# Performance work log

Hardware: AMD Instinct MI355X
Metric: run time of the kernel (lower is better)

Reference implementation:

```python
import jax, jax.numpy as jnp
import numpy as np
from jax import lax

B, C_IN, HC, H, W, K = 32, 32, 64, 64, 64, 3


def _conv(x, w, b):
    # x: [B,C,H,W], w: [O,I,K,K] -> [B,O,H,W] (stride 1, pad 1)
    y = lax.conv_general_dilated(x, w, window_strides=(1, 1), padding=[(1, 1), (1, 1)],
                                 dimension_numbers=("NCHW", "OIHW", "NCHW"))
    return y + b[None, :, None, None]


def setup_inputs() -> dict:
    key = jax.random.key(0)
    ks = jax.random.split(key, 20)
    d = {
        "x": jax.random.normal(ks[0], (B, C_IN, H, W), jnp.float32),
        "hidden_state": jax.random.normal(ks[1], (B, HC, H, W), jnp.float32),
        "cell_state": jax.random.normal(ks[2], (B, HC, H, W), jnp.float32),
    }
    sx = 1.0 / np.sqrt(C_IN * K * K)
    sh = 1.0 / np.sqrt(HC * K * K)
    names_x = ["w_xi", "w_xf", "w_xo", "w_xg"]
    names_h = ["w_hi", "w_hf", "w_ho", "w_hg"]
    for i, n in enumerate(names_x):
        d[n] = jax.random.uniform(ks[3 + i], (HC, C_IN, K, K), jnp.float32, -sx, sx)
        d["b" + n[1:]] = jax.random.uniform(ks[7 + i], (HC,), jnp.float32, -sx, sx)
    for i, n in enumerate(names_h):
        d[n] = jax.random.uniform(ks[11 + i], (HC, HC, K, K), jnp.float32, -sh, sh)
        d["b" + n[1:]] = jax.random.uniform(ks[15 + i], (HC,), jnp.float32, -sh, sh)
    return d


def reference(x, hidden_state, cell_state,
              w_xi, w_xf, w_xo, w_xg, b_xi, b_xf, b_xo, b_xg,
              w_hi, w_hf, w_ho, w_hg, b_hi, b_hf, b_ho, b_hg):
    Wx = jnp.concatenate([w_xi, w_xf, w_xo, w_xg], axis=0)
    bx = jnp.concatenate([b_xi, b_xf, b_xo, b_xg], axis=0)
    Wh = jnp.concatenate([w_hi, w_hf, w_ho, w_hg], axis=0)
    bh = jnp.concatenate([b_hi, b_hf, b_ho, b_hg], axis=0)
    gates = _conv(x, Wx, bx) + _conv(hidden_state, Wh, bh)  # [B,4*HC,H,W]
    zi, zf, zo, zg = jnp.split(gates, 4, axis=1)
    i = jax.nn.sigmoid(zi)
    f = jax.nn.sigmoid(zf)
    o = jax.nn.sigmoid(zo)
    g = jnp.tanh(zg)
    c_new = f * cell_state + i * g
    h_new = o * jnp.tanh(c_new)
    return (h_new, c_new)
```

## Files before the change

### kernel.cpp

```cpp
#include <hip/hip_runtime.h>


#define B_   32
#define CIN  32
#define HC_  64
#define HH   64
#define WW   64

#define A_ELEMS (9 * 6 * 8 * 64 * 8)
#define P_ROW   (12 * 66 * 8)
#define AKK     4096
#define BLDS    25344

typedef __attribute__((ext_vector_type(8)))  short  short8;
typedef __attribute__((ext_vector_type(16))) float  floatx16;

struct PackArgs {
    const float* wx[4]; const float* wh[4];
    const float* bx[4]; const float* bh[4];
};

__device__ __forceinline__ short f2bf(float f) {
    unsigned u = __float_as_uint(f);
    u += 0x7FFFu + ((u >> 16) & 1u);
    return (short)(u >> 16);
}

__device__ __forceinline__ void gl_lds16(const short* g, short* l) {
    __builtin_amdgcn_global_load_lds(
        (const __attribute__((address_space(1))) unsigned int*)g,
        (__attribute__((address_space(3))) unsigned int*)l, 16, 0, 0);
}

__global__ __launch_bounds__(256) void pack_weights(PackArgs pa, short* a_pk, float* bias) {
    int idx = blockIdx.x * 256 + threadIdx.x;
    if (idx < A_ELEMS) {
        int j    = idx & 7;
        int lane = (idx >> 3) & 63;
        int rest = idx >> 9;
        int s    = rest & 7;
        int rest2 = rest >> 3;
        int kk   = rest2 % 6;
        int tap  = rest2 / 6;
        int og = s >> 1, fi = s & 1;
        int m32 = lane & 31;
        int gate = 2 * fi + (m32 >> 4);
        int oc   = og * 16 + (m32 & 15);
        int c    = kk * 16 + (lane >> 5) * 8 + j;
        int ky = tap / 3, kx = tap - 3 * ky;
        float v = (c < CIN)
            ? pa.wx[gate][((oc * CIN + c) * 3 + ky) * 3 + kx]
            : pa.wh[gate][((oc * HC_ + (c - CIN)) * 3 + ky) * 3 + kx];
        a_pk[idx] = f2bf(v);
    }
    if (idx < 256) {
        int gate = idx >> 6, oc = idx & 63;
        bias[idx] = pa.bx[gate][oc] + pa.bh[gate][oc];
    }
}

__global__ __launch_bounds__(256) void pack_input(const float* __restrict__ x,
                                                  const float* __restrict__ h,
                                                  short* __restrict__ P) {
    const int yy = blockIdx.x, b = blockIdx.y;
    int4* prow4 = (int4*)(P + ((size_t)b * 66 + yy) * P_ROW);

    if (yy == 0 || yy == 65) {
        int4 z = {0, 0, 0, 0};
        for (int g = threadIdx.x; g < 792; g += 256) prow4[g] = z;
        return;
    }

    __shared__ short t[64 * 98];
    const int y = yy - 1;
    const int col = threadIdx.x & 63, cg = threadIdx.x >> 6;
    for (int c = cg; c < 96; c += 4) {
        float v = (c < CIN) ? x[((b * CIN + c) * HH + y) * WW + col]
                            : h[((b * HC_ + (c - CIN)) * HH + y) * WW + col];
        t[col * 98 + c] = f2bf(v);
    }
    __syncthreads();

    for (int g = threadIdx.x; g < 792; g += 256) {
        int pc = g / 66, xx = g - 66 * pc;
        int4 val = {0, 0, 0, 0};
        if (xx >= 1 && xx <= 64) {
            const short* sp = &t[(xx - 1) * 98 + pc * 8];
            val.x = *(const int*)(sp + 0); val.y = *(const int*)(sp + 2);
            val.z = *(const int*)(sp + 4); val.w = *(const int*)(sp + 6);
        }
        prow4[g] = val;
    }
}

__global__ __launch_bounds__(512, 4) void convlstm_main(
    const short* __restrict__ P, const short* __restrict__ a_pk,
    const float* __restrict__ bias, const float* __restrict__ cell,
    float* __restrict__ out)
{
    __shared__ __align__(16) short lds[BLDS];

    const int tid = threadIdx.x;
    const int b  = blockIdx.x >> 5;
    const int y0 = (blockIdx.x & 31) * 2;

    const int wv = tid >> 6, lane = tid & 63;
    const int ln31 = lane & 31, hg = lane >> 5;
    const int og = wv & 3, nh = wv >> 2;
    const int y = y0 + nh;

    floatx16 acc[2][2];
    #pragma unroll
    for (int fi = 0; fi < 2; ++fi)
        #pragma unroll
        for (int ns = 0; ns < 2; ++ns)
            #pragma unroll
            for (int q = 0; q < 16; ++q) acc[fi][ns][q] = 0.f;

    const short* Ag  = a_pk + og * 1024 + lane * 8;
    const int    b_rd = nh * 6336 + hg * 528 + ln31 * 8;

    {
        const short* Bsrc = P + ((size_t)(b * 66) + y0) * P_ROW;
        #pragma unroll
        for (int i = 0; i < 7; ++i) {
            int id = i * 512 + tid;
            if (id < 3168)
                gl_lds16(Bsrc + id * 8, lds + (i * 512 + wv * 64) * 8);
        }
    }
    __syncthreads();

    for (int tap = 0; tap < 9; ++tap) {
        const int ky = tap / 3, kx = tap % 3;
        const short* Bb = lds + b_rd + ky * 6336 + kx * 8;
        const short* Ac = Ag + tap * 6 * AKK;

        #pragma unroll
        for (int kk = 0; kk < 6; ++kk) {
            short8 a0 = *(const short8*)&Ac[kk * AKK];
            short8 a1 = *(const short8*)&Ac[kk * AKK + 512];
            short8 b0 = *(const short8*)&Bb[kk * 1056];
            short8 b1 = *(const short8*)&Bb[kk * 1056 + 256];
            acc[0][0] = __builtin_amdgcn_mfma_f32_32x32x16_bf16(a0, b0, acc[0][0], 0, 0, 0);
            acc[0][1] = __builtin_amdgcn_mfma_f32_32x32x16_bf16(a0, b1, acc[0][1], 0, 0, 0);
            acc[1][0] = __builtin_amdgcn_mfma_f32_32x32x16_bf16(a1, b0, acc[1][0], 0, 0, 0);
            acc[1][1] = __builtin_amdgcn_mfma_f32_32x32x16_bf16(a1, b1, acc[1][1], 0, 0, 0);
        }
    }

    const size_t plane = (size_t)B_ * HC_ * HH * WW;
    #pragma unroll
    for (int q = 0; q < 4; ++q)
    #pragma unroll
    for (int b8 = 0; b8 < 2; ++b8) {
        const int oc16 = q + 4 * hg + 8 * b8;
        const int oc = og * 16 + oc16;
        const float Bi = bias[oc],       Bf = bias[64 + oc];
        const float Bo = bias[128 + oc], Bg = bias[192 + oc];
        const int r_lo = q + 4 * b8, r_hi = q + 4 * (2 + b8);
        #pragma unroll
        for (int ns = 0; ns < 2; ++ns) {
            float zi = acc[0][ns][r_lo] + Bi;
            float zf = acc[0][ns][r_hi] + Bf;
            float zo = acc[1][ns][r_lo] + Bo;
            float zg = acc[1][ns][r_hi] + Bg;
            float ig = 1.f / (1.f + __expf(-zi));
            float fg = 1.f / (1.f + __expf(-zf));
            float sg = 1.f / (1.f + __expf(-zo));
            float e2 = __expf(2.f * zg);
            float gg = 1.f - 2.f / (e2 + 1.f);
            const int x = ns * 32 + ln31;
            size_t off = ((size_t)(b * HC_ + oc) * HH + y) * WW + x;
            float cn = fg * cell[off] + ig * gg;
            float ec = __expf(2.f * cn);
            out[off] = sg * (1.f - 2.f / (ec + 1.f));
            out[plane + off] = cn;
        }
    }
}

extern "C" void kernel_launch(void* const* d_in, const int* in_sizes, int n_in,
                              void* d_out, int out_size, void* d_ws, size_t ws_size,
                              hipStream_t stream) {
    PackArgs pa;
    pa.wx[0] = (const float*)d_in[3];  pa.bx[0] = (const float*)d_in[4];
    pa.wx[1] = (const float*)d_in[5];  pa.bx[1] = (const float*)d_in[6];
    pa.wx[2] = (const float*)d_in[7];  pa.bx[2] = (const float*)d_in[8];
    pa.wx[3] = (const float*)d_in[9];  pa.bx[3] = (const float*)d_in[10];
    pa.wh[0] = (const float*)d_in[11]; pa.bh[0] = (const float*)d_in[12];
    pa.wh[1] = (const float*)d_in[13]; pa.bh[1] = (const float*)d_in[14];
    pa.wh[2] = (const float*)d_in[15]; pa.bh[2] = (const float*)d_in[16];
    pa.wh[3] = (const float*)d_in[17]; pa.bh[3] = (const float*)d_in[18];

    short* a_pk = (short*)d_ws;
    float* bias = (float*)((char*)d_ws + A_ELEMS * sizeof(short));
    short* P    = (short*)((char*)d_ws + 443392);

    pack_weights<<<dim3(A_ELEMS / 256), dim3(256), 0, stream>>>(pa, a_pk, bias);
    pack_input <<<dim3(66, B_), dim3(256), 0, stream>>>(
        (const float*)d_in[0], (const float*)d_in[1], P);
    convlstm_main<<<dim3(B_ * 32), dim3(512), 0, stream>>>(
        P, a_pk, bias, (const float*)d_in[2], (float*)d_out);
}
```

Measured before the change: 245.8 us.

## Stage weights through triple-buffered LDS and stream input rows per kernel row

```diff
diff --git a/kernel.cpp b/kernel.cpp
--- a/kernel.cpp
+++ b/kernel.cpp
@@ -9,8 +9,8 @@
 
 #define A_ELEMS (9 * 6 * 8 * 64 * 8)
 #define P_ROW   (12 * 66 * 8)
-#define AKK     4096
-#define BLDS    25344
+#define ACH     8192
+#define BROWS   12672
 
 typedef __attribute__((ext_vector_type(8)))  short  short8;
 typedef __attribute__((ext_vector_type(16))) float  floatx16;
@@ -98,7 +98,7 @@
     const float* __restrict__ bias, const float* __restrict__ cell,
     float* __restrict__ out)
 {
-    __shared__ __align__(16) short lds[BLDS];
+    __shared__ __align__(16) short lds[BROWS + 3 * ACH];
 
     const int tid = threadIdx.x;
     const int b  = blockIdx.x >> 5;
@@ -117,37 +117,76 @@
             #pragma unroll
             for (int q = 0; q < 16; ++q) acc[fi][ns][q] = 0.f;
 
-    const short* Ag  = a_pk + og * 1024 + lane * 8;
-    const int    b_rd = nh * 6336 + hg * 528 + ln31 * 8;
-
-    {
-        const short* Bsrc = P + ((size_t)(b * 66) + y0) * P_ROW;
+    short* ldsB = lds;
+    short* As   = lds + BROWS;
+
+    const int a_rd = og * 1024 + lane * 8;
+    const int b_rd = nh * 6336 + hg * 528 + ln31 * 8;
+
+    #define STAGE_B(KY) do {                                                   \
+        const short* Bs_ = P + ((size_t)(b * 66) + y0 + (KY)) * P_ROW;         \
+        _Pragma("unroll")                                                      \
+        for (int i_ = 0; i_ < 3; ++i_)                                         \
+            gl_lds16(Bs_ + (i_ * 512 + tid) * 8, ldsB + (i_ * 512 + wv * 64) * 8); \
+        if (tid >= 464)                                                        \
+            gl_lds16(Bs_ + (1520 + lane) * 8, ldsB + 1520 * 8);                \
+    } while (0)
+
+    #define STAGE_A(C) do {                                                    \
+        const short* s_ = a_pk + (C) * ACH;                                    \
+        short* d_ = As + ((C) % 3) * ACH;                                      \
+        _Pragma("unroll")                                                      \
+        for (int i_ = 0; i_ < 2; ++i_)                                         \
+            gl_lds16(s_ + (i_ * 512 + tid) * 8, d_ + (i_ * 512 + wv * 64) * 8);\
+    } while (0)
+
+    STAGE_B(0);
+    STAGE_A(0);
+    STAGE_A(1);
+    asm volatile("s_waitcnt vmcnt(2)" ::: "memory");
+    __builtin_amdgcn_s_barrier();
+    __builtin_amdgcn_sched_barrier(0);
+
+    #pragma unroll
+    for (int c = 0; c < 27; ++c) {
+        const int tap = c / 3, ky = tap / 3, kx = tap % 3;
+        const bool bdry = (c == 9 || c == 18);
+
+        if (bdry) STAGE_B(ky);
+        if (c < 25) STAGE_A(c + 2);
+        if (bdry) {
+            asm volatile("s_waitcnt vmcnt(2)" ::: "memory");
+            __builtin_amdgcn_s_barrier();
+            __builtin_amdgcn_sched_barrier(0);
+        }
+
+        const short* Ab = As + (c % 3) * ACH + a_rd;
+        const short* Bb = ldsB + b_rd + kx * 8;
+
         #pragma unroll
-        for (int i = 0; i < 7; ++i) {
-            int id = i * 512 + tid;
-            if (id < 3168)
-                gl_lds16(Bsrc + id * 8, lds + (i * 512 + wv * 64) * 8);
-        }
-    }
-    __syncthreads();
-
-    for (int tap = 0; tap < 9; ++tap) {
-        const int ky = tap / 3, kx = tap % 3;
-        const short* Bb = lds + b_rd + ky * 6336 + kx * 8;
-        const short* Ac = Ag + tap * 6 * AKK;
-
-        #pragma unroll
-        for (int kk = 0; kk < 6; ++kk) {
-            short8 a0 = *(const short8*)&Ac[kk * AKK];
-            short8 a1 = *(const short8*)&Ac[kk * AKK + 512];
+        for (int kkl = 0; kkl < 2; ++kkl) {
+            const int kk = 2 * (c % 3) + kkl;
+            short8 a0 = *(const short8*)&Ab[kkl * 4096];
+            short8 a1 = *(const short8*)&Ab[kkl * 4096 + 512];
             short8 b0 = *(const short8*)&Bb[kk * 1056];
             short8 b1 = *(const short8*)&Bb[kk * 1056 + 256];
+            __builtin_amdgcn_s_setprio(1);
             acc[0][0] = __builtin_amdgcn_mfma_f32_32x32x16_bf16(a0, b0, acc[0][0], 0, 0, 0);
             acc[0][1] = __builtin_amdgcn_mfma_f32_32x32x16_bf16(a0, b1, acc[0][1], 0, 0, 0);
             acc[1][0] = __builtin_amdgcn_mfma_f32_32x32x16_bf16(a1, b0, acc[1][0], 0, 0, 0);
             acc[1][1] = __builtin_amdgcn_mfma_f32_32x32x16_bf16(a1, b1, acc[1][1], 0, 0, 0);
-        }
-    }
+            __builtin_amdgcn_s_setprio(0);
+        }
+
+        if (c < 25)       asm volatile("s_waitcnt vmcnt(2)" ::: "memory");
+        else if (c == 25) asm volatile("s_waitcnt vmcnt(0)" ::: "memory");
+        if (c < 26) {
+            __builtin_amdgcn_s_barrier();
+            __builtin_amdgcn_sched_barrier(0);
+        }
+    }
+    #undef STAGE_A
+    #undef STAGE_B
 
     const size_t plane = (size_t)B_ * HC_ * HH * WW;
     #pragma unroll
```

Measured after the change: 227.0 us. 7.6% less time.

## Stream weights through per-wave LDS ring with async loads; one row per block

Applied to the files above, without the earlier changes.

```diff
diff --git a/kernel.cpp b/kernel.cpp
--- a/kernel.cpp
+++ b/kernel.cpp
@@ -9,8 +9,8 @@
 
 #define A_ELEMS (9 * 6 * 8 * 64 * 8)
 #define P_ROW   (12 * 66 * 8)
-#define AKK     4096
-#define BLDS    25344
+#define BLDS    (3 * P_ROW)
+#define ARING   1024
 
 typedef __attribute__((ext_vector_type(8)))  short  short8;
 typedef __attribute__((ext_vector_type(16))) float  floatx16;
@@ -93,21 +93,20 @@
     }
 }
 
-__global__ __launch_bounds__(512, 4) void convlstm_main(
+__global__ __launch_bounds__(256, 2) void convlstm_main(
     const short* __restrict__ P, const short* __restrict__ a_pk,
     const float* __restrict__ bias, const float* __restrict__ cell,
     float* __restrict__ out)
 {
-    __shared__ __align__(16) short lds[BLDS];
+    __shared__ __align__(16) short lds[BLDS + 4 * 4 * ARING];
 
     const int tid = threadIdx.x;
-    const int b  = blockIdx.x >> 5;
-    const int y0 = (blockIdx.x & 31) * 2;
+    const int b = blockIdx.x >> 6;
+    const int y = blockIdx.x & 63;
 
     const int wv = tid >> 6, lane = tid & 63;
     const int ln31 = lane & 31, hg = lane >> 5;
-    const int og = wv & 3, nh = wv >> 2;
-    const int y = y0 + nh;
+    const int og = wv;
 
     floatx16 acc[2][2];
     #pragma unroll
@@ -117,36 +116,57 @@
             #pragma unroll
             for (int q = 0; q < 16; ++q) acc[fi][ns][q] = 0.f;
 
-    const short* Ag  = a_pk + og * 1024 + lane * 8;
-    const int    b_rd = nh * 6336 + hg * 528 + ln31 * 8;
+    short* Aring = lds + BLDS + wv * (4 * ARING);
+    const int b_rd = hg * 528 + ln31 * 8;
 
     {
-        const short* Bsrc = P + ((size_t)(b * 66) + y0) * P_ROW;
-        #pragma unroll
-        for (int i = 0; i < 7; ++i) {
-            int id = i * 512 + tid;
-            if (id < 3168)
-                gl_lds16(Bsrc + id * 8, lds + (i * 512 + wv * 64) * 8);
+        const short* Bsrc = P + ((size_t)(b * 66) + y) * P_ROW;
+        #pragma unroll
+        for (int i = 0; i < 10; ++i) {
+            int id = i * 256 + tid;
+            if (id < 2376)
+                gl_lds16(Bsrc + id * 8, lds + (i * 256 + wv * 64) * 8);
+        }
+        #pragma unroll
+        for (int ck = 0; ck < 3; ++ck) {
+            const short* src = a_pk + ck * 4096 + og * 1024 + lane * 8;
+            gl_lds16(src,       Aring + ck * ARING);
+            gl_lds16(src + 512, Aring + ck * ARING + 512);
         }
     }
     __syncthreads();
 
-    for (int tap = 0; tap < 9; ++tap) {
+    #pragma unroll
+    for (int c = 0; c < 54; ++c) {
+        const int tap = c / 6, kk = c % 6;
         const int ky = tap / 3, kx = tap % 3;
-        const short* Bb = lds + b_rd + ky * 6336 + kx * 8;
-        const short* Ac = Ag + tap * 6 * AKK;
-
-        #pragma unroll
-        for (int kk = 0; kk < 6; ++kk) {
-            short8 a0 = *(const short8*)&Ac[kk * AKK];
-            short8 a1 = *(const short8*)&Ac[kk * AKK + 512];
-            short8 b0 = *(const short8*)&Bb[kk * 1056];
-            short8 b1 = *(const short8*)&Bb[kk * 1056 + 256];
-            acc[0][0] = __builtin_amdgcn_mfma_f32_32x32x16_bf16(a0, b0, acc[0][0], 0, 0, 0);
-            acc[0][1] = __builtin_amdgcn_mfma_f32_32x32x16_bf16(a0, b1, acc[0][1], 0, 0, 0);
-            acc[1][0] = __builtin_amdgcn_mfma_f32_32x32x16_bf16(a1, b0, acc[1][0], 0, 0, 0);
-            acc[1][1] = __builtin_amdgcn_mfma_f32_32x32x16_bf16(a1, b1, acc[1][1], 0, 0, 0);
-        }
+
+        if (c < 51) {
+            const short* src = a_pk + (c + 3) * 4096 + og * 1024 + lane * 8;
+            short* dst = Aring + ((c + 3) & 3) * ARING;
+            gl_lds16(src,       dst);
+            gl_lds16(src + 512, dst + 512);
+        }
+
+        if (c < 51)       asm volatile("s_waitcnt vmcnt(6)" ::: "memory");
+        else if (c == 51) asm volatile("s_waitcnt vmcnt(4)" ::: "memory");
+        else if (c == 52) asm volatile("s_waitcnt vmcnt(2)" ::: "memory");
+        else              asm volatile("s_waitcnt vmcnt(0)" ::: "memory");
+
+        const short* Ab = Aring + (c & 3) * ARING + lane * 8;
+        const short* Bb = lds + b_rd + ky * 6336 + kk * 1056 + kx * 8;
+
+        short8 a0 = *(const short8*)&Ab[0];
+        short8 a1 = *(const short8*)&Ab[512];
+        short8 b0 = *(const short8*)&Bb[0];
+        short8 b1 = *(const short8*)&Bb[256];
+
+        __builtin_amdgcn_s_setprio(1);
+        acc[0][0] = __builtin_amdgcn_mfma_f32_32x32x16_bf16(a0, b0, acc[0][0], 0, 0, 0);
+        acc[0][1] = __builtin_amdgcn_mfma_f32_32x32x16_bf16(a0, b1, acc[0][1], 0, 0, 0);
+        acc[1][0] = __builtin_amdgcn_mfma_f32_32x32x16_bf16(a1, b0, acc[1][0], 0, 0, 0);
+        acc[1][1] = __builtin_amdgcn_mfma_f32_32x32x16_bf16(a1, b1, acc[1][1], 0, 0, 0);
+        __builtin_amdgcn_s_setprio(0);
     }
 
     const size_t plane = (size_t)B_ * HC_ * HH * WW;
@@ -200,6 +220,6 @@
     pack_weights<<<dim3(A_ELEMS / 256), dim3(256), 0, stream>>>(pa, a_pk, bias);
     pack_input <<<dim3(66, B_), dim3(256), 0, stream>>>(
         (const float*)d_in[0], (const float*)d_in[1], P);
-    convlstm_main<<<dim3(B_ * 32), dim3(512), 0, stream>>>(
+    convlstm_main<<<dim3(B_ * 64), dim3(256), 0, stream>>>(
         P, a_pk, bias, (const float*)d_in[2], (float*)d_out);
 }
```

New measurement: 226.9 us. 7.7% less time.

## Merge packing kernels and software-pipeline weight loads in the conv main loop

Applied to the files above, without the earlier changes.

```diff
diff --git a/kernel.cpp b/kernel.cpp
--- a/kernel.cpp
+++ b/kernel.cpp
@@ -9,8 +9,7 @@
 
 #define A_ELEMS (9 * 6 * 8 * 64 * 8)
 #define P_ROW   (12 * 66 * 8)
-#define AKK     4096
-#define BLDS    25344
+#define BLDS    (4 * P_ROW)
 
 typedef __attribute__((ext_vector_type(8)))  short  short8;
 typedef __attribute__((ext_vector_type(16))) float  floatx16;
@@ -32,37 +31,42 @@
         (__attribute__((address_space(3))) unsigned int*)l, 16, 0, 0);
 }
 
-__global__ __launch_bounds__(256) void pack_weights(PackArgs pa, short* a_pk, float* bias) {
-    int idx = blockIdx.x * 256 + threadIdx.x;
-    if (idx < A_ELEMS) {
-        int j    = idx & 7;
-        int lane = (idx >> 3) & 63;
-        int rest = idx >> 9;
-        int s    = rest & 7;
-        int rest2 = rest >> 3;
-        int kk   = rest2 % 6;
-        int tap  = rest2 / 6;
-        int og = s >> 1, fi = s & 1;
-        int m32 = lane & 31;
-        int gate = 2 * fi + (m32 >> 4);
-        int oc   = og * 16 + (m32 & 15);
-        int c    = kk * 16 + (lane >> 5) * 8 + j;
-        int ky = tap / 3, kx = tap - 3 * ky;
-        float v = (c < CIN)
-            ? pa.wx[gate][((oc * CIN + c) * 3 + ky) * 3 + kx]
-            : pa.wh[gate][((oc * HC_ + (c - CIN)) * 3 + ky) * 3 + kx];
-        a_pk[idx] = f2bf(v);
-    }
-    if (idx < 256) {
-        int gate = idx >> 6, oc = idx & 63;
-        bias[idx] = pa.bx[gate][oc] + pa.bh[gate][oc];
-    }
-}
-
-__global__ __launch_bounds__(256) void pack_input(const float* __restrict__ x,
-                                                  const float* __restrict__ h,
-                                                  short* __restrict__ P) {
-    const int yy = blockIdx.x, b = blockIdx.y;
+__global__ __launch_bounds__(256) void pack_all(PackArgs pa, short* a_pk, float* bias,
+                                                const float* __restrict__ x,
+                                                const float* __restrict__ h,
+                                                short* __restrict__ P) {
+    __shared__ short t[64 * 98];
+
+    if (blockIdx.x < 864) {
+        int idx = blockIdx.x * 256 + threadIdx.x;
+        {
+            int j    = idx & 7;
+            int lane = (idx >> 3) & 63;
+            int rest = idx >> 9;
+            int s    = rest & 7;
+            int rest2 = rest >> 3;
+            int kk   = rest2 % 6;
+            int tap  = rest2 / 6;
+            int og = s >> 1, fi = s & 1;
+            int m32 = lane & 31;
+            int gate = 2 * fi + (m32 >> 4);
+            int oc   = og * 16 + (m32 & 15);
+            int c    = kk * 16 + (lane >> 5) * 8 + j;
+            int ky = tap / 3, kx = tap - 3 * ky;
+            float v = (c < CIN)
+                ? pa.wx[gate][((oc * CIN + c) * 3 + ky) * 3 + kx]
+                : pa.wh[gate][((oc * HC_ + (c - CIN)) * 3 + ky) * 3 + kx];
+            a_pk[idx] = f2bf(v);
+        }
+        if (idx < 256) {
+            int gate = idx >> 6, oc = idx & 63;
+            bias[idx] = pa.bx[gate][oc] + pa.bh[gate][oc];
+        }
+        return;
+    }
+
+    const int bb = blockIdx.x - 864;
+    const int yy = bb % 66, b = bb / 66;
     int4* prow4 = (int4*)(P + ((size_t)b * 66 + yy) * P_ROW);
 
     if (yy == 0 || yy == 65) {
@@ -71,7 +75,6 @@
         return;
     }
 
-    __shared__ short t[64 * 98];
     const int y = yy - 1;
     const int col = threadIdx.x & 63, cg = threadIdx.x >> 6;
     for (int c = cg; c < 96; c += 4) {
@@ -117,8 +120,7 @@
             #pragma unroll
             for (int q = 0; q < 16; ++q) acc[fi][ns][q] = 0.f;
 
-    const short* Ag  = a_pk + og * 1024 + lane * 8;
-    const int    b_rd = nh * 6336 + hg * 528 + ln31 * 8;
+    const int b_rd = nh * 6336 + hg * 528 + ln31 * 8;
 
     {
         const short* Bsrc = P + ((size_t)(b * 66) + y0) * P_ROW;
@@ -129,24 +131,36 @@
                 gl_lds16(Bsrc + id * 8, lds + (i * 512 + wv * 64) * 8);
         }
     }
+
+    const short* Ab = a_pk + og * 1024 + lane * 8;
+    short8 ar[3][2];
+    #pragma unroll
+    for (int s = 0; s < 3; ++s) {
+        ar[s][0] = *(const short8*)(Ab + s * 4096);
+        ar[s][1] = *(const short8*)(Ab + s * 4096 + 512);
+    }
     __syncthreads();
 
-    for (int tap = 0; tap < 9; ++tap) {
+    #pragma unroll
+    for (int c = 0; c < 54; ++c) {
+        const int tap = c / 6, kk = c % 6;
         const int ky = tap / 3, kx = tap % 3;
-        const short* Bb = lds + b_rd + ky * 6336 + kx * 8;
-        const short* Ac = Ag + tap * 6 * AKK;
-
-        #pragma unroll
-        for (int kk = 0; kk < 6; ++kk) {
-            short8 a0 = *(const short8*)&Ac[kk * AKK];
-            short8 a1 = *(const short8*)&Ac[kk * AKK + 512];
-            short8 b0 = *(const short8*)&Bb[kk * 1056];
-            short8 b1 = *(const short8*)&Bb[kk * 1056 + 256];
-            acc[0][0] = __builtin_amdgcn_mfma_f32_32x32x16_bf16(a0, b0, acc[0][0], 0, 0, 0);
-            acc[0][1] = __builtin_amdgcn_mfma_f32_32x32x16_bf16(a0, b1, acc[0][1], 0, 0, 0);
-            acc[1][0] = __builtin_amdgcn_mfma_f32_32x32x16_bf16(a1, b0, acc[1][0], 0, 0, 0);
-            acc[1][1] = __builtin_amdgcn_mfma_f32_32x32x16_bf16(a1, b1, acc[1][1], 0, 0, 0);
-        }
+
+        short8 a0 = ar[c % 3][0];
+        short8 a1 = ar[c % 3][1];
+        if (c < 51) {
+            ar[c % 3][0] = *(const short8*)(Ab + (c + 3) * 4096);
+            ar[c % 3][1] = *(const short8*)(Ab + (c + 3) * 4096 + 512);
+        }
+
+        const short* Bb = lds + b_rd + ky * 6336 + kk * 1056 + kx * 8;
+        short8 b0 = *(const short8*)&Bb[0];
+        short8 b1 = *(const short8*)&Bb[256];
+
+        acc[0][0] = __builtin_amdgcn_mfma_f32_32x32x16_bf16(a0, b0, acc[0][0], 0, 0, 0);
+        acc[0][1] = __builtin_amdgcn_mfma_f32_32x32x16_bf16(a0, b1, acc[0][1], 0, 0, 0);
+        acc[1][0] = __builtin_amdgcn_mfma_f32_32x32x16_bf16(a1, b0, acc[1][0], 0, 0, 0);
+        acc[1][1] = __builtin_amdgcn_mfma_f32_32x32x16_bf16(a1, b1, acc[1][1], 0, 0, 0);
     }
 
     const size_t plane = (size_t)B_ * HC_ * HH * WW;
@@ -197,8 +211,8 @@
     float* bias = (float*)((char*)d_ws + A_ELEMS * sizeof(short));
     short* P    = (short*)((char*)d_ws + 443392);
 
-    pack_weights<<<dim3(A_ELEMS / 256), dim3(256), 0, stream>>>(pa, a_pk, bias);
-    pack_input <<<dim3(66, B_), dim3(256), 0, stream>>>(
+    pack_all<<<dim3(864 + 66 * B_), dim3(256), 0, stream>>>(
+        pa, a_pk, bias,
         (const float*)d_in[0], (const float*)d_in[1], P);
     convlstm_main<<<dim3(B_ * 32), dim3(512), 0, stream>>>(
         P, a_pk, bias, (const float*)d_in[2], (float*)d_out);
```

New measurement: 257.5 us. +4.8%, slower.
